# Kernel optimization log

Hardware: AMD Instinct MI355X
Metric: run time of the kernel (lower is better)

The kernel has to match this reference:

```python
import jax, jax.numpy as jnp
import numpy as np

B = 16384       # batch
H = 512         # hidden_size
OUT = 4         # output_size (== GRU input_size)
FF = 2048       # MLP hidden width
HORIZON = 5     # prediction_horizon


def setup_inputs() -> dict:
    key = jax.random.key(0)
    ks = jax.random.split(key, 12)
    s = 0.05
    f32 = jnp.float32
    return {
        "predicted_values": jax.random.normal(ks[0], (B, HORIZON, OUT), f32),
        "past_time_features": jax.random.normal(ks[1], (B, H), f32),
        # nn.GRU (single layer) params, PyTorch layout: (3H, in) / (3H, H), gate order r,z,n
        "w_ih": jax.random.normal(ks[2], (3 * H, OUT), f32) * s,
        "w_hh": jax.random.normal(ks[3], (3 * H, H), f32) * s,
        "b_ih": jax.random.normal(ks[4], (3 * H,), f32) * s,
        "b_hh": jax.random.normal(ks[5], (3 * H,), f32) * s,
        # hx_fc: Linear(2H -> H)
        "w_fc": jax.random.normal(ks[6], (H, 2 * H), f32) * s,
        "b_fc": jax.random.normal(ks[7], (H,), f32) * s,
        # mlp: Linear(H -> 2048), Linear(2048 -> OUT); Dropout is identity at eval
        "w1": jax.random.normal(ks[8], (FF, H), f32) * s,
        "b1": jax.random.normal(ks[9], (FF,), f32) * s,
        "w2": jax.random.normal(ks[10], (OUT, FF), f32) * s,
        "b2": jax.random.normal(ks[11], (OUT,), f32) * s,
    }


def _gru_cell(x, h, w_ih, w_hh, b_ih, b_hh):
    # PyTorch GRU cell: gates ordered (r, z, n)
    gi = x @ w_ih.T + b_ih          # [B, 3H]
    gh = h @ w_hh.T + b_hh          # [B, 3H]
    i_r, i_z, i_n = jnp.split(gi, 3, axis=-1)
    h_r, h_z, h_n = jnp.split(gh, 3, axis=-1)
    r = jax.nn.sigmoid(i_r + h_r)
    z = jax.nn.sigmoid(i_z + h_z)
    n = jnp.tanh(i_n + r * h_n)
    return (1.0 - z) * n + z * h


def reference(predicted_values, past_time_features, w_ih, w_hh, b_ih, b_hh,
              w_fc, b_fc, w1, b1, w2, b2):
    b = predicted_values.shape[0]
    xy = jnp.zeros((b, OUT), predicted_values.dtype)
    hx = past_time_features.reshape(b, H)
    outs = []
    for i in range(HORIZON):
        # length-2 sequence through the GRU: [xy, predicted_values[:, i]]
        h1 = _gru_cell(xy, hx, w_ih, w_hh, b_ih, b_hh)
        h2 = _gru_cell(predicted_values[:, i, :], h1, w_ih, w_hh, b_ih, b_hh)
        hcat = jnp.concatenate([h1, h2], axis=-1)        # [B, 2H]
        hx = hcat @ w_fc.T + b_fc                        # [B, H]
        # MLP: ReLU -> Linear -> (Dropout=identity) -> ReLU -> Linear
        d_xy = jax.nn.relu(jax.nn.relu(hx) @ w1.T + b1) @ w2.T + b2
        xy = xy + d_xy
        outs.append(xy)
    return jnp.stack(outs, axis=1)                       # [B, HORIZON, OUT]
```

## Files before the change

### kernel.cpp

```cpp
#include <hip/hip_runtime.h>
#include <hip/hip_bf16.h>
#include <cstdint>
#include <cstddef>

#define Bsz 16384
#define HORsz 5

using bf16_t = __hip_bfloat16;
typedef __bf16 bf16x8 __attribute__((ext_vector_type(8)));
typedef float f32x4 __attribute__((ext_vector_type(4)));

__device__ __forceinline__ void gld_lds16(const void* g, void* l) {
  __builtin_amdgcn_global_load_lds((__attribute__((address_space(1))) void*)g,
                                   (__attribute__((address_space(3))) void*)l,
                                   16, 0, 0);
}

__device__ __forceinline__ float sigm(float x) { return 1.f / (1.f + __expf(-x)); }
__device__ __forceinline__ float tanh_fast(float x) {
  x = fminf(fmaxf(x, -20.f), 20.f);
  float e = __expf(2.f * x);
  return (e - 1.f) / (e + 1.f);
}

__device__ __forceinline__ void swz(int b, int nbn, int& n, int& m) {
  const int x = b & 7;
  const int k = b >> 3;
  n = k % nbn;
  m = x + 8 * (k / nbn);
}

__device__ __forceinline__ size_t fl_off(int row, int col, int ca, int cofs) {
  return (size_t)((row >> 4) * ca + cofs + (col >> 5)) * 1024
       + (size_t)((((col >> 3) & 3) * 16 + (row & 15)) * 16 + (col & 7) * 2);
}

__global__ void __launch_bounds__(256) pack_fl(const float* __restrict__ src,
                                               char* __restrict__ dst,
                                               int C, int cs, int npieces) {
  const int p = blockIdx.x * 256 + threadIdx.x;
  if (p >= npieces) return;
  const int chunk = p >> 6, wi = p & 63;
  const int colgrp = wi >> 4, r15 = wi & 15;
  const int rowgrp = chunk >> cs, kg = chunk & ((1 << cs) - 1);
  const int row = rowgrp * 16 + r15;
  const int col = kg * 32 + colgrp * 8;
  const float* s = src + (size_t)row * C + col;
  bf16x8 v;
  #pragma unroll
  for (int j = 0; j < 8; ++j) v[j] = (__bf16)s[j];
  *(bf16x8*)(dst + (size_t)p * 16) = v;
}

__global__ void __launch_bounds__(256, 3) gru_fused4(
    const char* __restrict__ Afl, int ca,
    const char* __restrict__ Wfl,
    const float* __restrict__ x, int ldx,
    const float* __restrict__ w_ih, const float* __restrict__ b_ih,
    const float* __restrict__ b_hh,
    char* __restrict__ Ofl, int co, int kofs)
{
  __shared__ char smem[32768];
  const int t = threadIdx.x, w = t >> 6, lane = t & 63;
  int bn, bm;
  swz(blockIdx.x, 8, bn, bm);
  const int m0 = bm * 64;
  const int n0 = bn * 64;

  const char* gsrc[4];
  int loff[4];
  #pragma unroll
  for (int s = 0; s < 4; ++s) {
    const int idx = w * 4 + s;
    if (idx < 4) {
      gsrc[s] = Afl + (size_t)((m0 >> 4) + idx) * ca * 1024 + lane * 16;
    } else {
      const int c = idx - 4, g = c >> 2, cr = c & 3;
      gsrc[s] = Wfl + (size_t)(g * 32 + (n0 >> 4) + cr) * 16 * 1024 + lane * 16;
    }
    loff[s] = idx * 1024;
  }

  f32x4 acc[3][4];
  const f32x4 zero = {0.f, 0.f, 0.f, 0.f};
  #pragma unroll
  for (int g = 0; g < 3; ++g)
    #pragma unroll
    for (int i = 0; i < 4; ++i) acc[g][i] = zero;

  #pragma unroll
  for (int s = 0; s < 4; ++s)
    gld_lds16(gsrc[s], smem + loff[s]);

  #pragma unroll
  for (int kg = 0; kg < 16; ++kg) {
    __syncthreads();
    const char* cur = smem + (kg & 1) * 16384;
    if (kg + 1 < 16) {
      char* nxt = smem + ((kg + 1) & 1) * 16384;
      #pragma unroll
      for (int s = 0; s < 4; ++s)
        gld_lds16(gsrc[s] + (size_t)(kg + 1) * 1024, nxt + loff[s]);
    }
    bf16x8 af[4];
    #pragma unroll
    for (int i = 0; i < 4; ++i)
      af[i] = *(const bf16x8*)(cur + i * 1024 + lane * 16);
    #pragma unroll
    for (int g = 0; g < 3; ++g) {
      const bf16x8 bv = *(const bf16x8*)(cur + (4 + g * 4 + w) * 1024 + lane * 16);
      #pragma unroll
      for (int i = 0; i < 4; ++i)
        acc[g][i] = __builtin_amdgcn_mfma_f32_16x16x32_bf16(af[i], bv, acc[g][i], 0, 0, 0);
    }
  }

  const int lr = lane & 15, q4 = (lane >> 4) * 4;
  char* rep = smem + w * 2048;
  const int c = n0 + w * 16 + lr;
  const float4 wr  = *(const float4*)(w_ih + (size_t)c * 4);
  const float4 wz  = *(const float4*)(w_ih + (size_t)(c + 512) * 4);
  const float4 wnn = *(const float4*)(w_ih + (size_t)(c + 1024) * 4);
  const float bir = b_ih[c], biz = b_ih[c + 512], bin = b_ih[c + 1024];
  const float bhr = b_hh[c], bhz = b_hh[c + 512], bhn = b_hh[c + 1024];
  const int wbase = ((lr >> 3) * 16 + q4) * 16 + (lr & 7) * 2;
  #pragma unroll
  for (int i = 0; i < 4; ++i) {
    #pragma unroll
    for (int r4 = 0; r4 < 4; ++r4) {
      const int row = m0 + i * 16 + q4 + r4;
      const float4 xv = *(const float4*)(x + (size_t)row * ldx);
      const float gir = bir + xv.x * wr.x  + xv.y * wr.y  + xv.z * wr.z  + xv.w * wr.w;
      const float giz = biz + xv.x * wz.x  + xv.y * wz.y  + xv.z * wz.z  + xv.w * wz.w;
      const float gin = bin + xv.x * wnn.x + xv.y * wnn.y + xv.z * wnn.z + xv.w * wnn.w;
      const float rr = sigm(gir + acc[0][i][r4] + bhr);
      const float zz = sigm(giz + acc[1][i][r4] + bhz);
      const float nn = tanh_fast(gin + rr * (acc[2][i][r4] + bhn));
      const float hp = (float)*(const __bf16*)(Afl + fl_off(row, c, ca, 0));
      *(__bf16*)(rep + i * 512 + wbase + r4 * 16) = (__bf16)((1.f - zz) * nn + zz * hp);
    }
  }
  const int rg0 = m0 >> 4;
  const int cg = kofs + (n0 >> 5) + (w >> 1);
  const int half = (w & 1) * 512;
  #pragma unroll
  for (int i = 0; i < 4; ++i) {
    const uint2 v = *(const uint2*)(rep + i * 512 + lane * 8);
    *(uint2*)(Ofl + ((size_t)(rg0 + i) * co + cg) * 1024 + half + lane * 8) = v;
  }
}

template <int NKG, int NJ, int MODE>
__global__ void __launch_bounds__(256, 4) gemm_fl5(
    const char* __restrict__ Afl,
    const char* __restrict__ Bfl, int nbn,
    const float* __restrict__ bias,
    char* __restrict__ O1, char* __restrict__ O2, int co,
    const float* __restrict__ w2, float* __restrict__ dxy)
{
  constexpr int NCH = 8 + 2 * NJ;
  constexpr int NS = NCH / 4;
  constexpr int BUFB = NCH * 1024;
  __shared__ char smem[2 * BUFB];
  const int t = threadIdx.x, w = t >> 6, lane = t & 63;
  int bn, bm;
  swz(blockIdx.x, nbn, bn, bm);
  const int m0 = bm * 128, n0 = bn * (NJ * 32);
  const int wm = (w >> 1) * 64, wn = (w & 1) * (NJ * 16);

  const char* gsrc[NS];
  int loff[NS];
  #pragma unroll
  for (int s = 0; s < NS; ++s) {
    const int idx = w * NS + s;
    if (idx < 8) gsrc[s] = Afl + (size_t)((m0 >> 4) + idx) * NKG * 1024 + lane * 16;
    else         gsrc[s] = Bfl + (size_t)((n0 >> 4) + idx - 8) * NKG * 1024 + lane * 16;
    loff[s] = idx * 1024;
  }

  f32x4 acc[4][NJ];
  const f32x4 zero = {0.f, 0.f, 0.f, 0.f};
  #pragma unroll
  for (int i = 0; i < 4; ++i)
    #pragma unroll
    for (int j = 0; j < NJ; ++j) acc[i][j] = zero;

  #pragma unroll
  for (int s = 0; s < NS; ++s)
    gld_lds16(gsrc[s], smem + loff[s]);

  #pragma unroll
  for (int kg = 0; kg < NKG; ++kg) {
    __syncthreads();
    const char* cur = smem + (kg & 1) * BUFB;
    if (kg + 1 < NKG) {
      char* nxt = smem + ((kg + 1) & 1) * BUFB;
      #pragma unroll
      for (int s = 0; s < NS; ++s)
        gld_lds16(gsrc[s] + (size_t)(kg + 1) * 1024, nxt + loff[s]);
    }
    bf16x8 af[4], bv[NJ];
    #pragma unroll
    for (int i = 0; i < 4; ++i)
      af[i] = *(const bf16x8*)(cur + ((wm >> 4) + i) * 1024 + lane * 16);
    #pragma unroll
    for (int j = 0; j < NJ; ++j)
      bv[j] = *(const bf16x8*)(cur + (8 + (wn >> 4) + j) * 1024 + lane * 16);
    #pragma unroll
    for (int i = 0; i < 4; ++i)
      #pragma unroll
      for (int j = 0; j < NJ; ++j)
        acc[i][j] = __builtin_amdgcn_mfma_f32_16x16x32_bf16(af[i], bv[j], acc[i][j], 0, 0, 0);
  }

  const int lr = lane & 15, q4 = (lane >> 4) * 4;
  if (MODE == 2) {
    char* rep = smem + w * (NJ / 2) * 1024;
    const int rgb = (m0 >> 4) + (wm >> 4);
    const int cgb = (n0 >> 5) + (wn >> 5);
    for (int i = 0; i < 4; ++i) {
      #pragma unroll
      for (int j = 0; j < NJ; ++j) {
        const int col = n0 + wn + j * 16 + lr;
        const float bvv = bias[col];
        const int wbase = (((j & 1) * 2 + (lr >> 3)) * 16 + q4) * 16 + (lr & 7) * 2;
        #pragma unroll
        for (int r = 0; r < 4; ++r) {
          const float v = acc[i][j][r] + bvv;
          *(__bf16*)(rep + (j >> 1) * 1024 + wbase + r * 16) = (__bf16)v;
        }
      }
      #pragma unroll
      for (int jc = 0; jc < NJ / 2; ++jc) {
        const bf16x8 v = *(const bf16x8*)(rep + jc * 1024 + lane * 16);
        const size_t cb = ((size_t)(rgb + i) * co + cgb + jc) * 1024 + lane * 16;
        *(bf16x8*)(O1 + cb) = v;
        bf16x8 vr;
        #pragma unroll
        for (int e = 0; e < 8; ++e) vr[e] = (__bf16)fmaxf((float)v[e], 0.f);
        *(bf16x8*)(O2 + cb) = vr;
      }
    }
  } else {
    const int slice = bn * 2 + (w & 1);
    #pragma unroll
    for (int i = 0; i < 4; ++i) {
      float v[4][4];
      #pragma unroll
      for (int r = 0; r < 4; ++r)
        #pragma unroll
        for (int o = 0; o < 4; ++o) v[r][o] = 0.f;
      #pragma unroll
      for (int j = 0; j < NJ; ++j) {
        const int col = n0 + wn + j * 16 + lr;
        const float bvv = bias[col];
        const float w20 = w2[col], w21 = w2[2048 + col], w22 = w2[4096 + col], w23 = w2[6144 + col];
        #pragma unroll
        for (int r = 0; r < 4; ++r) {
          const float pv = fmaxf(acc[i][j][r] + bvv, 0.f);
          v[r][0] += pv * w20; v[r][1] += pv * w21; v[r][2] += pv * w22; v[r][3] += pv * w23;
        }
      }
      #pragma unroll
      for (int m = 1; m <= 8; m <<= 1)
        #pragma unroll
        for (int r = 0; r < 4; ++r)
          #pragma unroll
          for (int o = 0; o < 4; ++o) v[r][o] += __shfl_xor(v[r][o], m);
      if (lr == 0) {
        #pragma unroll
        for (int r = 0; r < 4; ++r) {
          const int row = m0 + wm + i * 16 + q4 + r;
          float4 vv = make_float4(v[r][0], v[r][1], v[r][2], v[r][3]);
          *(float4*)(dxy + ((size_t)slice * Bsz + row) * 4) = vv;
        }
      }
    }
  }
}

__global__ void __launch_bounds__(256) finalize(
    const float* __restrict__ dxy, const float* __restrict__ b2,
    float* __restrict__ xy, float* __restrict__ out, int istep)
{
  const int b = blockIdx.x * 256 + threadIdx.x;
  float4 s = *(const float4*)b2;
  #pragma unroll 8
  for (int sl = 0; sl < 32; ++sl) {
    const float4 d = *(const float4*)(dxy + ((size_t)sl * Bsz + b) * 4);
    s.x += d.x; s.y += d.y; s.z += d.z; s.w += d.w;
  }
  float4 xv = *(const float4*)(xy + (size_t)b * 4);
  xv.x += s.x; xv.y += s.y; xv.z += s.z; xv.w += s.w;
  *(float4*)(xy + (size_t)b * 4) = xv;
  *(float4*)(out + (size_t)b * 20 + istep * 4) = xv;
}

extern "C" void kernel_launch(void* const* d_in, const int* in_sizes, int n_in,
                              void* d_out, int out_size, void* d_ws, size_t ws_size,
                              hipStream_t stream)
{
  const float* pv   = (const float*)d_in[0];
  const float* ptf  = (const float*)d_in[1];
  const float* w_ih = (const float*)d_in[2];
  const float* w_hh = (const float*)d_in[3];
  const float* b_ih = (const float*)d_in[4];
  const float* b_hh = (const float*)d_in[5];
  const float* w_fc = (const float*)d_in[6];
  const float* b_fc = (const float*)d_in[7];
  const float* w1   = (const float*)d_in[8];
  const float* b1   = (const float*)d_in[9];
  const float* w2   = (const float*)d_in[10];
  const float* b2   = (const float*)d_in[11];
  float* out = (float*)d_out;

  char* p = (char*)d_ws;
  auto carve = [&](size_t bytes) {
    char* r = p;
    p += (bytes + 255) & ~(size_t)255;
    return r;
  };
  char*  hxF   = carve((size_t)Bsz * 512 * 2);
  char*  hxrF  = carve((size_t)Bsz * 512 * 2);
  char*  hcatF = carve((size_t)Bsz * 1024 * 2);
  float* dxy   = (float*)carve((size_t)32 * Bsz * 4 * 4);
  float* xy    = (float*)carve((size_t)Bsz * 4 * 4);
  char*  whhF  = carve((size_t)1536 * 512 * 2);
  char*  wfcF  = carve((size_t)512 * 1024 * 2);
  char*  w1F   = carve((size_t)2048 * 512 * 2);

  pack_fl<<<(1536 * 512 / 8 + 255) / 256, 256, 0, stream>>>(w_hh, whhF, 512, 4, 1536 * 512 / 8);
  pack_fl<<<(512 * 1024 / 8 + 255) / 256, 256, 0, stream>>>(w_fc, wfcF, 1024, 5, 512 * 1024 / 8);
  pack_fl<<<(2048 * 512 / 8 + 255) / 256, 256, 0, stream>>>(w1, w1F, 512, 4, 2048 * 512 / 8);
  pack_fl<<<(Bsz * 512 / 8 + 255) / 256, 256, 0, stream>>>(ptf, hxF, 512, 4, Bsz * 512 / 8);
  hipMemsetAsync(xy, 0, (size_t)Bsz * 4 * 4, stream);

  for (int i = 0; i < HORsz; ++i) {
    gru_fused4<<<2048, 256, 0, stream>>>(
        hxF, 16, whhF, xy, 4, w_ih, b_ih, b_hh, hcatF, 32, 0);
    gru_fused4<<<2048, 256, 0, stream>>>(
        hcatF, 32, whhF, pv + i * 4, HORsz * 4, w_ih, b_ih, b_hh, hcatF, 32, 16);
    gemm_fl5<32, 2, 2><<<1024, 256, 0, stream>>>(
        hcatF, wfcF, 8, b_fc, hxF, hxrF, 16, nullptr, nullptr);
    gemm_fl5<16, 4, 3><<<2048, 256, 0, stream>>>(
        hxrF, w1F, 16, b1, nullptr, nullptr, 0, w2, dxy);
    finalize<<<Bsz / 256, 256, 0, stream>>>(dxy, b2, xy, out, i);
  }
}
```

Measured before the change: 869.9 us.

## Add dedicated 256x256-tile MLP kernel and enlarge hx_fc GEMM tiles

Replaces the MLP path of the generic gemm_fl5 with a new 512-thread mlp2b kernel. It uses 256x256 output tiles, double-buffered LDS loads via global_load_lds, and s_setprio around the MFMA block, and fuses bias, ReLU and the w2 projection into 32 partial slices (unchanged count). The hx_fc GEMM template parameters also change to a larger tile with half the grid. Larger tiles raise arithmetic intensity and cut redundant global/LDS traffic, at the cost of more registers per thread and fewer blocks.

New measurement: 876.5 us. About the same (+0.8%).

```diff
diff --git a/kernel.cpp b/kernel.cpp
--- a/kernel.cpp
+++ b/kernel.cpp
@@ -241,39 +241,106 @@
         *(bf16x8*)(O2 + cb) = vr;
       }
     }
-  } else {
-    const int slice = bn * 2 + (w & 1);
-    #pragma unroll
-    for (int i = 0; i < 4; ++i) {
-      float v[4][4];
+  }
+}
+
+__global__ void __launch_bounds__(512, 2) mlp2b(
+    const char* __restrict__ Afl,
+    const char* __restrict__ Bfl,
+    const float* __restrict__ bias,
+    const float* __restrict__ w2,
+    float* __restrict__ dxy)
+{
+  __shared__ char smem[2 * 32768];
+  const int t = threadIdx.x, w = t >> 6, lane = t & 63;
+  const int wr = w >> 2, wc = w & 3;
+  int bn, bm;
+  swz(blockIdx.x, 8, bn, bm);
+  const int m0 = bm * 256, n0 = bn * 256;
+
+  const char* gsrc[4];
+  int loff[4];
+  #pragma unroll
+  for (int s = 0; s < 4; ++s) {
+    const int idx = w * 4 + s;
+    if (idx < 16) {
+      gsrc[s] = Afl + (size_t)((m0 >> 4) + idx) * 16 * 1024 + lane * 16;
+      loff[s] = idx * 1024;
+    } else {
+      gsrc[s] = Bfl + (size_t)((n0 >> 4) + idx - 16) * 16 * 1024 + lane * 16;
+      loff[s] = 16384 + (idx - 16) * 1024;
+    }
+  }
+
+  f32x4 acc[8][4];
+  const f32x4 zero = {0.f, 0.f, 0.f, 0.f};
+  #pragma unroll
+  for (int i = 0; i < 8; ++i)
+    #pragma unroll
+    for (int j = 0; j < 4; ++j) acc[i][j] = zero;
+
+  #pragma unroll
+  for (int s = 0; s < 4; ++s)
+    gld_lds16(gsrc[s], smem + loff[s]);
+
+  #pragma unroll
+  for (int kg = 0; kg < 16; ++kg) {
+    __syncthreads();
+    const char* cur = smem + (kg & 1) * 32768;
+    if (kg + 1 < 16) {
+      char* nxt = smem + ((kg + 1) & 1) * 32768;
+      #pragma unroll
+      for (int s = 0; s < 4; ++s)
+        gld_lds16(gsrc[s] + (size_t)(kg + 1) * 1024, nxt + loff[s]);
+    }
+    bf16x8 af[8], bv[4];
+    #pragma unroll
+    for (int j = 0; j < 4; ++j)
+      bv[j] = *(const bf16x8*)(cur + 16384 + (wc * 4 + j) * 1024 + lane * 16);
+    #pragma unroll
+    for (int i = 0; i < 8; ++i)
+      af[i] = *(const bf16x8*)(cur + (wr * 8 + i) * 1024 + lane * 16);
+    __builtin_amdgcn_s_setprio(1);
+    #pragma unroll
+    for (int i = 0; i < 8; ++i)
+      #pragma unroll
+      for (int j = 0; j < 4; ++j)
+        acc[i][j] = __builtin_amdgcn_mfma_f32_16x16x32_bf16(af[i], bv[j], acc[i][j], 0, 0, 0);
+    __builtin_amdgcn_s_setprio(0);
+  }
+
+  const int lr = lane & 15, q4 = (lane >> 4) * 4;
+  const int slice = bn * 4 + wc;
+  #pragma unroll
+  for (int i = 0; i < 8; ++i) {
+    float v[4][4];
+    #pragma unroll
+    for (int r = 0; r < 4; ++r)
+      #pragma unroll
+      for (int o = 0; o < 4; ++o) v[r][o] = 0.f;
+    #pragma unroll
+    for (int j = 0; j < 4; ++j) {
+      const int col = n0 + wc * 64 + j * 16 + lr;
+      const float bvv = bias[col];
+      const float w20 = w2[col], w21 = w2[2048 + col], w22 = w2[4096 + col], w23 = w2[6144 + col];
+      #pragma unroll
+      for (int r = 0; r < 4; ++r) {
+        const float pv = fmaxf(acc[i][j][r] + bvv, 0.f);
+        v[r][0] += pv * w20; v[r][1] += pv * w21; v[r][2] += pv * w22; v[r][3] += pv * w23;
+      }
+    }
+    #pragma unroll
+    for (int m = 1; m <= 8; m <<= 1)
       #pragma unroll
       for (int r = 0; r < 4; ++r)
         #pragma unroll
-        for (int o = 0; o < 4; ++o) v[r][o] = 0.f;
-      #pragma unroll
-      for (int j = 0; j < NJ; ++j) {
-        const int col = n0 + wn + j * 16 + lr;
-        const float bvv = bias[col];
-        const float w20 = w2[col], w21 = w2[2048 + col], w22 = w2[4096 + col], w23 = w2[6144 + col];
-        #pragma unroll
-        for (int r = 0; r < 4; ++r) {
-          const float pv = fmaxf(acc[i][j][r] + bvv, 0.f);
-          v[r][0] += pv * w20; v[r][1] += pv * w21; v[r][2] += pv * w22; v[r][3] += pv * w23;
-        }
-      }
-      #pragma unroll
-      for (int m = 1; m <= 8; m <<= 1)
-        #pragma unroll
-        for (int r = 0; r < 4; ++r)
-          #pragma unroll
-          for (int o = 0; o < 4; ++o) v[r][o] += __shfl_xor(v[r][o], m);
-      if (lr == 0) {
-        #pragma unroll
-        for (int r = 0; r < 4; ++r) {
-          const int row = m0 + wm + i * 16 + q4 + r;
-          float4 vv = make_float4(v[r][0], v[r][1], v[r][2], v[r][3]);
-          *(float4*)(dxy + ((size_t)slice * Bsz + row) * 4) = vv;
-        }
+        for (int o = 0; o < 4; ++o) v[r][o] += __shfl_xor(v[r][o], m);
+    if (lr == 0) {
+      #pragma unroll
+      for (int r = 0; r < 4; ++r) {
+        const int row = m0 + wr * 128 + i * 16 + q4 + r;
+        float4 vv = make_float4(v[r][0], v[r][1], v[r][2], v[r][3]);
+        *(float4*)(dxy + ((size_t)slice * Bsz + row) * 4) = vv;
       }
     }
   }
@@ -340,10 +407,9 @@
         hxF, 16, whhF, xy, 4, w_ih, b_ih, b_hh, hcatF, 32, 0);
     gru_fused4<<<2048, 256, 0, stream>>>(
         hcatF, 32, whhF, pv + i * 4, HORsz * 4, w_ih, b_ih, b_hh, hcatF, 32, 16);
-    gemm_fl5<32, 2, 2><<<1024, 256, 0, stream>>>(
-        hcatF, wfcF, 8, b_fc, hxF, hxrF, 16, nullptr, nullptr);
-    gemm_fl5<16, 4, 3><<<2048, 256, 0, stream>>>(
-        hxrF, w1F, 16, b1, nullptr, nullptr, 0, w2, dxy);
+    gemm_fl5<32, 4, 2><<<512, 256, 0, stream>>>(
+        hcatF, wfcF, 4, b_fc, hxF, hxrF, 16, nullptr, nullptr);
+    mlp2b<<<512, 512, 0, stream>>>(hxrF, w1F, b1, w2, dxy);
     finalize<<<Bsz / 256, 256, 0, stream>>>(dxy, b2, xy, out, i);
   }
 }
```
